# Kernel tuning notes

Hardware: AMD Instinct MI355X
Metric: run time of the kernel (lower is better)

Reference implementation:

```python
import jax, jax.numpy as jnp
import numpy as np

B, C, H, W = 8, 64, 128, 128
G, DGPG = 4, 1
GD = G * DGPG          # total deformable groups = 4
COUT = 64
KH = KW = 3
K = KH * KW            # 9 kernel locations
PAD = STR = DIL = 1
HO, WO = 128, 128      # same padding, stride 1
OFFSET_SCALE = 1.0
CDG = C // GD          # channels per deformable group = 16
CPG = C // G           # input channels per conv group = 16
KOFF = 7
POFF = 3


def dwconv7(x, w, b):
    # depthwise 7x7 conv, groups == channels; w: [C,1,7,7]
    y = jax.lax.conv_general_dilated(
        x, w, window_strides=(1, 1), padding=[(POFF, POFF), (POFF, POFF)],
        feature_group_count=C, dimension_numbers=('NCHW', 'OIHW', 'NCHW'))
    return y + b[None, :, None, None]


def gn1(x, g, b):
    # GroupNorm with a single group: normalize over (C,H,W) per sample
    m = x.mean(axis=(1, 2, 3), keepdims=True)
    v = x.var(axis=(1, 2, 3), keepdims=True)
    return (x - m) * jax.lax.rsqrt(v + 1e-5) * g[None, :, None, None] + b[None, :, None, None]


def pw(x, w, b):
    # 1x1 conv; w: [O, C]
    return jnp.einsum('bchw,oc->bohw', x, w) + b[None, :, None, None]


def setup_inputs() -> dict:
    key = jax.random.key(0)
    ks = jax.random.split(key, 8)
    s = 0.02
    return {
        'x': jax.random.normal(ks[0], (B, C, H, W), jnp.float32),
        'w_dw_off': jax.random.normal(ks[1], (C, 1, KOFF, KOFF), jnp.float32) * s,
        'b_dw_off': jnp.zeros((C,), jnp.float32),
        'gn_off_g': jnp.ones((C,), jnp.float32),
        'gn_off_b': jnp.zeros((C,), jnp.float32),
        'w_pw_off': jax.random.normal(ks[2], (GD * K * 2, C), jnp.float32) * s,
        'b_pw_off': jnp.zeros((GD * K * 2,), jnp.float32),
        'w_dw_m': jax.random.normal(ks[3], (C, 1, KOFF, KOFF), jnp.float32) * s,
        'b_dw_m': jnp.zeros((C,), jnp.float32),
        'gn_m_g': jnp.ones((C,), jnp.float32),
        'gn_m_b': jnp.zeros((C,), jnp.float32),
        'w_pw_m': jax.random.normal(ks[4], (GD * K, C), jnp.float32) * s,
        'b_pw_m': jnp.zeros((GD * K,), jnp.float32),
        'weight': jax.random.normal(ks[5], (COUT, CPG, KH, KW), jnp.float32) * s,
        'bias': jax.random.normal(ks[6], (COUT,), jnp.float32) * s,
    }


def _deform_conv(x, offset, mask, weight, bias):
    # offset: [B, GD, K, 2, HO, WO] (y, x); mask: [B, GD, K, HO, WO] (softmaxed)
    ky, kx = jnp.meshgrid(jnp.arange(KH), jnp.arange(KW), indexing='ij')
    ky = ky.reshape(K).astype(x.dtype)
    kx = kx.reshape(K).astype(x.dtype)
    oy = jnp.arange(HO, dtype=x.dtype)
    ox = jnp.arange(WO, dtype=x.dtype)
    base_y = oy[None, :] * STR - PAD + ky[:, None] * DIL   # [K, HO]
    base_x = ox[None, :] * STR - PAD + kx[:, None] * DIL   # [K, WO]
    py = base_y[None, None, :, :, None] + offset[:, :, :, 0] * OFFSET_SCALE  # [B,GD,K,HO,WO]
    px = base_x[None, None, :, None, :] + offset[:, :, :, 1] * OFFSET_SCALE

    x_flat = x.reshape(B, GD, CDG, H * W)
    y0 = jnp.floor(py)
    x0 = jnp.floor(px)
    wy = py - y0
    wx = px - x0

    def gather(yi, xi):
        valid = ((yi >= 0) & (yi < H) & (xi >= 0) & (xi < W)).astype(x.dtype)
        yc = jnp.clip(yi, 0, H - 1).astype(jnp.int32)
        xc = jnp.clip(xi, 0, W - 1).astype(jnp.int32)
        idx = (yc * W + xc).reshape(B, GD, 1, K * HO * WO)
        v = jnp.take_along_axis(x_flat, idx, axis=3).reshape(B, GD, CDG, K, HO, WO)
        return v * valid[:, :, None]

    v = (gather(y0, x0) * ((1 - wy) * (1 - wx))[:, :, None]
         + gather(y0, x0 + 1) * ((1 - wy) * wx)[:, :, None]
         + gather(y0 + 1, x0) * (wy * (1 - wx))[:, :, None]
         + gather(y0 + 1, x0 + 1) * (wy * wx)[:, :, None])
    v = v * mask[:, :, None]                               # modulated samples
    v = v.reshape(B, G, CPG, K, HO, WO)
    wg = weight.reshape(G, COUT // G, CPG, K)
    out = jnp.einsum('bgckhw,gock->bgohw', v, wg).reshape(B, COUT, HO, WO)
    return out + bias[None, :, None, None]


def reference(x, w_dw_off, b_dw_off, gn_off_g, gn_off_b, w_pw_off, b_pw_off,
              w_dw_m, b_dw_m, gn_m_g, gn_m_b, w_pw_m, b_pw_m, weight, bias):
    off = pw(gn1(dwconv7(x, w_dw_off, b_dw_off), gn_off_g, gn_off_b), w_pw_off, b_pw_off)
    m = pw(gn1(dwconv7(x, w_dw_m, b_dw_m), gn_m_g, gn_m_b), w_pw_m, b_pw_m)
    offset = off.reshape(B, GD, K, 2, HO, WO)
    mask = jax.nn.softmax(m.reshape(B, GD, K, HO, WO), axis=2)  # attn over kernel points
    return _deform_conv(x, offset, mask, weight, bias)
```

## Files before the change

kernel.cpp:

```cpp
#include <hip/hip_runtime.h>
#include <hip/hip_fp16.h>
#include <math.h>

#define HW     16384
#define IMG_H  128
#define IMG_W  128

typedef _Float16 f16x2 __attribute__((ext_vector_type(2)));
typedef __fp16 fp16v2 __attribute__((ext_vector_type(2)));
typedef _Float16 f16x4 __attribute__((ext_vector_type(4)));
typedef float f32x4 __attribute__((ext_vector_type(4)));

#define OFF_T2    ((size_t)0)
#define OFF_XT    ((size_t)8388608)
#define OFF_WT    ((size_t)12582912)
#define OFF_PART  ((size_t)12599040)
#define OFF_AD    ((size_t)12631808)
#define OFF_WB    ((size_t)19711744)
#define OFF_WDW2  ((size_t)19716352)
#define OFF_WF2   ((size_t)19719936)
#define OFF_DC    ((size_t)19775232)

__global__ void k_prep(const float* __restrict__ wpw_off,
                       const float* __restrict__ wpw_m,
                       const float* __restrict__ wdef,
                       const float* __restrict__ wdwo,
                       const float* __restrict__ wdwm,
                       float* __restrict__ ws) {
    int i = blockIdx.x * 256 + threadIdx.x;
    if (i < 6912) {
        int c = i / 108, o = i % 108;
        ws[OFF_WT + i] = (o < 72) ? wpw_off[o * 64 + c] : wpw_m[(o - 72) * 64 + c];
    } else if (i < 9216) {
        int j = i - 6912;
        int lane = j & 63;
        int gt = j >> 6;
        int tap = gt % 9, g = gt / 9;
        int oc = lane & 15, qh = lane >> 4;
        union { ushort h[4]; uint2 u; } pk;
#pragma unroll
        for (int jj = 0; jj < 4; ++jj) {
            float wv = wdef[((g * 16 + oc) * 16 + (4 * qh + jj)) * 9 + tap];
            pk.h[jj] = __half_as_ushort(__float2half(wv));
        }
        ((uint2*)(ws + OFF_WB))[j] = pk.u;
    } else if (i < 12800) {
        int j = i - 9216;
        int q = j & 3;
        int r = j >> 2;
        int dy = r % 7;
        int cv = (r / 7) & 1;
        int c = r / 14;
        const float* src = cv ? wdwm : wdwo;
        int dx0 = q * 2;
        float w0 = src[c * 49 + dy * 7 + dx0];
        float w1 = (dx0 + 1 < 7) ? src[c * 49 + dy * 7 + dx0 + 1] : 0.f;
        union { __half h[2]; uint u; } pk;
        pk.h[0] = __float2half(w0);
        pk.h[1] = __float2half(w1);
        ((uint*)(ws + OFF_WDW2))[j] = pk.u;
    }
}

__global__ __launch_bounds__(256) void k_trans(const float* __restrict__ x,
                                               __half* __restrict__ xT) {
    int n = blockIdx.x * 256 + threadIdx.x;
    int p = n & (HW - 1);
    int bg = n >> 14;
    const float* src = x + (size_t)bg * 16 * HW + p;
    union { __half2 h2[8]; uint4 u[2]; } pk;
#pragma unroll
    for (int i = 0; i < 8; ++i) {
        float a = src[(size_t)(2 * i) * HW];
        float bq = src[(size_t)(2 * i + 1) * HW];
        pk.h2[i] = __halves2half2(__float2half(a), __float2half(bq));
    }
    uint4* dst = (uint4*)(xT + (size_t)n * 16);
    dst[0] = pk.u[0];
    dst[1] = pk.u[1];
}

__global__ __launch_bounds__(256) void k_dw(const float* __restrict__ x,
                                            const float* __restrict__ bdwo,
                                            const float* __restrict__ bdwm,
                                            const uint* __restrict__ wdw2,
                                            __half2* __restrict__ t2,
                                            float* __restrict__ partial) {
    int bid = blockIdx.x;
    int plane = bid >> 4;
    int stripe = (bid & 15) * 8;
    int t = threadIdx.x;
    int cb = t & 31;
    int row = stripe + (t >> 5);
    int c = plane & 63;
    const float4* pl = (const float4*)(x + (size_t)plane * HW);

    const uint* wp = wdw2 + c * 56;
    f16x2 wo2[7][4], wm2[7][4];
    union WU { uint u; f16x2 h; };
#pragma unroll
    for (int dy = 0; dy < 7; ++dy)
#pragma unroll
        for (int q = 0; q < 4; ++q) {
            WU a, bq;
            a.u = wp[dy * 4 + q];
            bq.u = wp[28 + dy * 4 + q];
            wo2[dy][q] = a.h;
            wm2[dy][q] = bq.h;
        }

    float acco[4] = {0.f, 0.f, 0.f, 0.f};
    float accm[4] = {0.f, 0.f, 0.f, 0.f};

    union CV { fp16v2 v; f16x2 h; };

#pragma unroll
    for (int dy = 0; dy < 7; ++dy) {
        int iy = row - 3 + dy;
        if (iy >= 0 && iy < IMG_H) {
            const float4* prow = pl + iy * 32;
            float4 f4 = prow[cb];
            float4 f4m = prow[cb == 0 ? 0 : cb - 1];
            float4 f4p = prow[cb == 31 ? 31 : cb + 1];
            bool le = (cb == 0), re = (cb == 31);
            float v[11];
            v[0] = le ? 0.f : f4m.y;
            v[1] = le ? 0.f : f4m.z;
            v[2] = le ? 0.f : f4m.w;
            v[3] = f4.x; v[4] = f4.y; v[5] = f4.z; v[6] = f4.w;
            v[7] = re ? 0.f : f4p.x;
            v[8] = re ? 0.f : f4p.y;
            v[9] = re ? 0.f : f4p.z;
            v[10] = re ? 0.f : f4p.w;
            f16x2 hp[10];
#pragma unroll
            for (int d = 0; d < 10; ++d) {
                CV cv;
                cv.v = __builtin_amdgcn_cvt_pkrtz(v[d], v[d + 1]);
                hp[d] = cv.h;
            }
#pragma unroll
            for (int cc = 0; cc < 4; ++cc) {
                float ao = acco[cc], am = accm[cc];
                ao = __builtin_amdgcn_fdot2(hp[cc],     wo2[dy][0], ao, false);
                ao = __builtin_amdgcn_fdot2(hp[cc + 2], wo2[dy][1], ao, false);
                ao = __builtin_amdgcn_fdot2(hp[cc + 4], wo2[dy][2], ao, false);
                ao = __builtin_amdgcn_fdot2(hp[cc + 6], wo2[dy][3], ao, false);
                am = __builtin_amdgcn_fdot2(hp[cc],     wm2[dy][0], am, false);
                am = __builtin_amdgcn_fdot2(hp[cc + 2], wm2[dy][1], am, false);
                am = __builtin_amdgcn_fdot2(hp[cc + 4], wm2[dy][2], am, false);
                am = __builtin_amdgcn_fdot2(hp[cc + 6], wm2[dy][3], am, false);
                acco[cc] = ao; accm[cc] = am;
            }
        }
    }

    float bo = bdwo[c], bm = bdwm[c];
    float s1o = 0.f, s2o = 0.f, s1m = 0.f, s2m = 0.f;
    union { __half2 h2[4]; uint4 u; } ot;
#pragma unroll
    for (int cc = 0; cc < 4; ++cc) {
        float vo = acco[cc] + bo, vm = accm[cc] + bm;
        ot.h2[cc] = __halves2half2(__float2half(vo), __float2half(vm));
        s1o += vo; s2o += vo * vo; s1m += vm; s2m += vm * vm;
    }
    *(uint4*)(t2 + (size_t)plane * HW + row * IMG_W + cb * 4) = ot.u;

#pragma unroll
    for (int d = 32; d; d >>= 1) {
        s1o += __shfl_down(s1o, d);
        s2o += __shfl_down(s2o, d);
        s1m += __shfl_down(s1m, d);
        s2m += __shfl_down(s2m, d);
    }
    __shared__ float red[4][4];
    if ((t & 63) == 0) {
        int w = t >> 6;
        red[w][0] = s1o; red[w][1] = s2o; red[w][2] = s1m; red[w][3] = s2m;
    }
    __syncthreads();
    if (t < 4) {
        float v = red[0][t] + red[1][t] + red[2][t] + red[3][t];
        partial[(size_t)bid * 4 + t] = v;
    }
}

__global__ __launch_bounds__(256) void k_fin(const float* __restrict__ partial,
                      const float* __restrict__ gog, const float* __restrict__ gob,
                      const float* __restrict__ gmg, const float* __restrict__ gmb,
                      float* __restrict__ ad) {
    int b = blockIdx.x, t = threadIdx.x;
    const float4* pp = (const float4*)partial + (size_t)b * 1024;
    float4 s = make_float4(0.f, 0.f, 0.f, 0.f);
#pragma unroll
    for (int i = 0; i < 4; ++i) {
        float4 v = pp[t + i * 256];
        s.x += v.x; s.y += v.y; s.z += v.z; s.w += v.w;
    }
#pragma unroll
    for (int d = 32; d; d >>= 1) {
        s.x += __shfl_down(s.x, d);
        s.y += __shfl_down(s.y, d);
        s.z += __shfl_down(s.z, d);
        s.w += __shfl_down(s.w, d);
    }
    __shared__ float red[4][4];
    if ((t & 63) == 0) {
        int w = t >> 6;
        red[w][0] = s.x; red[w][1] = s.y; red[w][2] = s.z; red[w][3] = s.w;
    }
    __syncthreads();
    if (t < 64) {
        float s1o = red[0][0] + red[1][0] + red[2][0] + red[3][0];
        float s2o = red[0][1] + red[1][1] + red[2][1] + red[3][1];
        float s1m = red[0][2] + red[1][2] + red[2][2] + red[3][2];
        float s2m = red[0][3] + red[1][3] + red[2][3] + red[3][3];
        int c = t;
        const float invN = 1.f / 1048576.f;
        float m_o = s1o * invN;
        float v_o = s2o * invN - m_o * m_o;
        float i_o = rsqrtf(v_o + 1e-5f);
        float m_m = s1m * invN;
        float v_m = s2m * invN - m_m * m_m;
        float i_m = rsqrtf(v_m + 1e-5f);
        float a_o = i_o * gog[c];
        float d_o = gob[c] - m_o * a_o;
        float a_m = i_m * gmg[c];
        float d_m = gmb[c] - m_m * a_m;
        ((float4*)ad)[b * 64 + c] = make_float4(a_o, d_o, a_m, d_m);
    }
}

__global__ __launch_bounds__(256) void k_fold(const float* __restrict__ wT,
                                              const float* __restrict__ ad,
                                              const float* __restrict__ bpo,
                                              const float* __restrict__ bpm,
                                              float* __restrict__ wf2,
                                              float* __restrict__ dconst) {
    int b = blockIdx.x, t = threadIdx.x;
    const float* adb = ad + b * 256;
    for (int i = t; i < 6912; i += 256) {
        int c = i / 108, o = i - c * 108;
        float a = (o < 72) ? adb[c * 4 + 0] : adb[c * 4 + 2];
        wf2[(size_t)b * 6912 + i] = a * wT[i];
    }
    if (t < 108) {
        float s = (t < 72) ? bpo[t] : bpm[t - 72];
        for (int c = 0; c < 64; ++c) {
            float d = (t < 72) ? adb[c * 4 + 1] : adb[c * 4 + 3];
            s = fmaf(d, wT[c * 108 + t], s);
        }
        dconst[b * 108 + t] = s;
    }
}

__global__ __launch_bounds__(256, 4) void k_gthf(const __half2* __restrict__ t2,
                                                 const float* __restrict__ wf2,
                                                 const float* __restrict__ dconst,
                                                 const __half* __restrict__ xT,
                                                 const uint2* __restrict__ wb,
                                                 const float* __restrict__ bias,
                                                 float* __restrict__ out) {
    __shared__ union SMem {
        struct {
            uint4 xsA[506];
            uint4 xsB[506];
            uint4 shv[768];
        } s;
        float shout[4864];
    } sm;

    int tid = threadIdx.x;
    int bid = blockIdx.x;
    int bg = bid & 31;
    int tile = bid >> 5;
    int tr = tile >> 3, tc = tile & 7;
    int r0 = tr * 16, c0 = tc * 16;
    int g = bg & 3, b = bg >> 2;
    int wr0 = r0 - 3, wc0 = c0 - 3;

    const __half* xg = xT + (size_t)bg * HW * 16;

#pragma unroll
    for (int it = 0; it < 2; ++it) {
        int idx = tid + it * 256;
        if (idx < 484) {
            int ly = idx / 22, lx = idx - ly * 22;
            int sr = wr0 + ly; sr = sr < 0 ? 0 : (sr > 127 ? 127 : sr);
            int sc = wc0 + lx; sc = sc < 0 ? 0 : (sc > 127 ? 127 : sc);
            const uint4* src = (const uint4*)(xg + (size_t)(sr * IMG_W + sc) * 16);
            sm.s.xsA[ly * 23 + lx] = src[0];
            sm.s.xsB[ly * 23 + lx] = src[1];
        }
    }

    int row = r0 + (tid >> 4), col = c0 + (tid & 15);
    int p = row * IMG_W + col;
    int lane = tid & 63, wv = tid >> 6;
    int m_idx = lane & 15, q_idx = lane >> 4;

    const float* dc = dconst + b * 108;
    float facc[18], macc[9];
#pragma unroll
    for (int o = 0; o < 18; ++o) facc[o] = dc[g * 18 + o];
#pragma unroll
    for (int o = 0; o < 9; ++o) macc[o] = dc[72 + g * 9 + o];

    const float* wfb = wf2 + (size_t)b * 6912;
    const __half2* tp = t2 + (size_t)b * 64 * HW + p;
#pragma unroll 8
    for (int c = 0; c < 64; ++c) {
        float2 tv = __half22float2(tp[(size_t)c * HW]);
        const float* wf = wfb + c * 108 + g * 18;
#pragma unroll
        for (int o = 0; o < 18; ++o) facc[o] = fmaf(wf[o], tv.x, facc[o]);
        const float* wm = wfb + c * 108 + 72 + g * 9;
#pragma unroll
        for (int o = 0; o < 9; ++o) macc[o] = fmaf(wm[o], tv.y, macc[o]);
    }
    {
        float mx = macc[0];
#pragma unroll
        for (int k = 1; k < 9; ++k) mx = fmaxf(mx, macc[k]);
        float s = 0.f;
#pragma unroll
        for (int k = 0; k < 9; ++k) {
            float e = __expf(macc[k] - mx);
            macc[k] = e;
            s += e;
        }
        float inv = 1.f / s;
#pragma unroll
        for (int k = 0; k < 9; ++k) macc[k] *= inv;
    }

    const uint2* wbp = wb + (size_t)(g * 9) * 64 + lane;
    f16x4 bfr[9];
    union BU { uint2 u; f16x4 h; };
#pragma unroll
    for (int k = 0; k < 9; ++k) { BU t; t.u = wbp[k * 64]; bfr[k] = t.h; }

    __syncthreads();

    uint4* shvw = sm.s.shv + tid * 3;
    const _Float16* shvh = (const _Float16*)sm.s.shv;

    f32x4 acc[4];
#pragma unroll
    for (int s = 0; s < 4; ++s) acc[s] = (f32x4){0.f, 0.f, 0.f, 0.f};

#pragma unroll
    for (int k = 0; k < 9; ++k) {
        float mk = macc[k];
        float py = (float)(row + k / 3 - 1) + facc[k * 2 + 0];
        float px = (float)(col + k % 3 - 1) + facc[k * 2 + 1];
        float y0f = floorf(py), x0f = floorf(px);
        float wy = py - y0f, wx = px - x0f;
        int iy0 = (int)y0f, ix0 = (int)x0f;
        int iy1 = iy0 + 1, ix1 = ix0 + 1;
        float fy0 = (iy0 >= 0 && iy0 < IMG_H) ? (1.f - wy) : 0.f;
        float fy1 = (iy1 >= 0 && iy1 < IMG_H) ? wy : 0.f;
        float fx0 = (ix0 >= 0 && ix0 < IMG_W) ? (1.f - wx) : 0.f;
        float fx1 = (ix1 >= 0 && ix1 < IMG_W) ? wx : 0.f;
        __half2 f00h = __float2half2_rn(fy0 * fx0 * mk);
        __half2 f01h = __float2half2_rn(fy0 * fx1 * mk);
        __half2 f10h = __float2half2_rn(fy1 * fx0 * mk);
        __half2 f11h = __float2half2_rn(fy1 * fx1 * mk);
        int ly0 = iy0 - wr0; ly0 = ly0 < 0 ? 0 : (ly0 > 21 ? 21 : ly0);
        int ly1 = iy1 - wr0; ly1 = ly1 < 0 ? 0 : (ly1 > 21 ? 21 : ly1);
        int lx0 = ix0 - wc0; lx0 = lx0 < 0 ? 0 : (lx0 > 21 ? 21 : lx0);
        int lx1 = ix1 - wc0; lx1 = lx1 < 0 ? 0 : (lx1 > 21 ? 21 : lx1);
        int i00 = ly0 * 23 + lx0, i01 = ly0 * 23 + lx1;
        int i10 = ly1 * 23 + lx0, i11 = ly1 * 23 + lx1;
        union Q8 { uint4 u[2]; __half2 h2[8]; };
        Q8 q00, q01, q10, q11;
        q00.u[0] = sm.s.xsA[i00]; q00.u[1] = sm.s.xsB[i00];
        q01.u[0] = sm.s.xsA[i01]; q01.u[1] = sm.s.xsB[i01];
        q10.u[0] = sm.s.xsA[i10]; q10.u[1] = sm.s.xsB[i10];
        q11.u[0] = sm.s.xsA[i11]; q11.u[1] = sm.s.xsB[i11];
        union V8 { __half2 h2[4]; uint4 u; };
        V8 pa, pb;
#pragma unroll
        for (int i = 0; i < 4; ++i) {
            __half2 vh = __hmul2(f00h, q00.h2[i]);
            vh = __hfma2(f01h, q01.h2[i], vh);
            vh = __hfma2(f10h, q10.h2[i], vh);
            vh = __hfma2(f11h, q11.h2[i], vh);
            pa.h2[i] = vh;
        }
#pragma unroll
        for (int i = 4; i < 8; ++i) {
            __half2 vh = __hmul2(f00h, q00.h2[i]);
            vh = __hfma2(f01h, q01.h2[i], vh);
            vh = __hfma2(f10h, q10.h2[i], vh);
            vh = __hfma2(f11h, q11.h2[i], vh);
            pb.h2[i - 4] = vh;
        }
        shvw[0] = pa.u;
        shvw[1] = pb.u;
#pragma unroll
        for (int s = 0; s < 4; ++s) {
            f16x4 af = *(const f16x4*)(shvh +
                        ((size_t)wv * 64 + s * 16 + m_idx) * 24 + q_idx * 4);
            acc[s] = __builtin_amdgcn_mfma_f32_16x16x16f16(af, bfr[k], acc[s], 0, 0, 0);
        }
    }

    __syncthreads();

#pragma unroll
    for (int s = 0; s < 4; ++s)
#pragma unroll
        for (int j = 0; j < 4; ++j)
            sm.shout[(wv * 64 + s * 16 + 4 * q_idx + j) * 19 + m_idx] = acc[s][j];

    float* outp = out + ((size_t)b * 64 + g * 16) * HW + p;
#pragma unroll
    for (int o = 0; o < 16; ++o)
        outp[(size_t)o * HW] = sm.shout[tid * 19 + o] + bias[g * 16 + o];
}

extern "C" void kernel_launch(void* const* d_in, const int* in_sizes, int n_in,
                              void* d_out, int out_size, void* d_ws, size_t ws_size,
                              hipStream_t stream) {
    const float* x        = (const float*)d_in[0];
    const float* w_dw_off = (const float*)d_in[1];
    const float* b_dw_off = (const float*)d_in[2];
    const float* gn_off_g = (const float*)d_in[3];
    const float* gn_off_b = (const float*)d_in[4];
    const float* w_pw_off = (const float*)d_in[5];
    const float* b_pw_off = (const float*)d_in[6];
    const float* w_dw_m   = (const float*)d_in[7];
    const float* b_dw_m   = (const float*)d_in[8];
    const float* gn_m_g   = (const float*)d_in[9];
    const float* gn_m_b   = (const float*)d_in[10];
    const float* w_pw_m   = (const float*)d_in[11];
    const float* b_pw_m   = (const float*)d_in[12];
    const float* weight   = (const float*)d_in[13];
    const float* bias     = (const float*)d_in[14];

    float* ws = (float*)d_ws;
    __half2* t2   = (__half2*)(ws + OFF_T2);
    __half* xT    = (__half*)(ws + OFF_XT);
    float* wT     = ws + OFF_WT;
    float* part   = ws + OFF_PART;
    float* adb    = ws + OFF_AD;
    const uint2* wb = (const uint2*)(ws + OFF_WB);
    const uint* wdw2 = (const uint*)(ws + OFF_WDW2);
    float* wf2    = ws + OFF_WF2;
    float* dconst = ws + OFF_DC;

    k_prep<<<50, 256, 0, stream>>>(w_pw_off, w_pw_m, weight, w_dw_off, w_dw_m, ws);
    k_trans<<<2048, 256, 0, stream>>>(x, xT);
    k_dw<<<8192, 256, 0, stream>>>(x, b_dw_off, b_dw_m, wdw2, t2, part);
    k_fin<<<8, 256, 0, stream>>>(part, gn_off_g, gn_off_b, gn_m_g, gn_m_b, adb);
    k_fold<<<8, 256, 0, stream>>>(wT, adb, b_pw_off, b_pw_m, wf2, dconst);
    k_gthf<<<2048, 256, 0, stream>>>(t2, wf2, dconst, xT, wb, bias, (float*)d_out);
}
```

Before: 112.6 us.

## Pack channel pairs in depthwise output and use fp16 dot2 for pointwise projection

The depthwise kernel now handles two channels per block and stores the offset and mask activations with channel pairs interleaved, as fp16x2 words. The folded pointwise weights are packed as fp16 pairs in a per-(batch, group) layout. This lets the gather kernel's 64-channel projection loop run as 32 fdot2 steps instead of 64 scalar FMA steps, which halves the number of strided activation loads and weight reads. The gather block order is also changed so blocks of the same batch-group run next to each other. In exchange the folded weights lose precision by moving from fp32 to fp16, and the depthwise kernel runs half as many blocks, each doing twice the work.

```diff
diff --git a/kernel.cpp b/kernel.cpp
--- a/kernel.cpp
+++ b/kernel.cpp
@@ -18,7 +18,7 @@
 #define OFF_AD    ((size_t)12631808)
 #define OFF_WB    ((size_t)19711744)
 #define OFF_WDW2  ((size_t)19716352)
-#define OFF_WF2   ((size_t)19719936)
+#define OFF_WPK   ((size_t)19719936)
 #define OFF_DC    ((size_t)19775232)
 
 __global__ void k_prep(const float* __restrict__ wpw_off,
@@ -84,87 +84,94 @@
                                             const float* __restrict__ bdwo,
                                             const float* __restrict__ bdwm,
                                             const uint* __restrict__ wdw2,
-                                            __half2* __restrict__ t2,
+                                            uint2* __restrict__ t2p,
                                             float* __restrict__ partial) {
     int bid = blockIdx.x;
-    int plane = bid >> 4;
+    int b = bid >> 9;
+    int c2 = (bid >> 4) & 31;
     int stripe = (bid & 15) * 8;
     int t = threadIdx.x;
     int cb = t & 31;
     int row = stripe + (t >> 5);
-    int c = plane & 63;
-    const float4* pl = (const float4*)(x + (size_t)plane * HW);
-
-    const uint* wp = wdw2 + c * 56;
-    f16x2 wo2[7][4], wm2[7][4];
+    int c0 = c2 * 2;
+
+    float vo[2][4], vm[2][4];
+    float s1o = 0.f, s2o = 0.f, s1m = 0.f, s2m = 0.f;
+    union CV { fp16v2 v; f16x2 h; };
     union WU { uint u; f16x2 h; };
-#pragma unroll
-    for (int dy = 0; dy < 7; ++dy)
-#pragma unroll
-        for (int q = 0; q < 4; ++q) {
-            WU a, bq;
-            a.u = wp[dy * 4 + q];
-            bq.u = wp[28 + dy * 4 + q];
-            wo2[dy][q] = a.h;
-            wm2[dy][q] = bq.h;
-        }
-
-    float acco[4] = {0.f, 0.f, 0.f, 0.f};
-    float accm[4] = {0.f, 0.f, 0.f, 0.f};
-
-    union CV { fp16v2 v; f16x2 h; };
-
-#pragma unroll
-    for (int dy = 0; dy < 7; ++dy) {
-        int iy = row - 3 + dy;
-        if (iy >= 0 && iy < IMG_H) {
-            const float4* prow = pl + iy * 32;
-            float4 f4 = prow[cb];
-            float4 f4m = prow[cb == 0 ? 0 : cb - 1];
-            float4 f4p = prow[cb == 31 ? 31 : cb + 1];
-            bool le = (cb == 0), re = (cb == 31);
-            float v[11];
-            v[0] = le ? 0.f : f4m.y;
-            v[1] = le ? 0.f : f4m.z;
-            v[2] = le ? 0.f : f4m.w;
-            v[3] = f4.x; v[4] = f4.y; v[5] = f4.z; v[6] = f4.w;
-            v[7] = re ? 0.f : f4p.x;
-            v[8] = re ? 0.f : f4p.y;
-            v[9] = re ? 0.f : f4p.z;
-            v[10] = re ? 0.f : f4p.w;
-            f16x2 hp[10];
-#pragma unroll
-            for (int d = 0; d < 10; ++d) {
-                CV cv;
-                cv.v = __builtin_amdgcn_cvt_pkrtz(v[d], v[d + 1]);
-                hp[d] = cv.h;
+
+#pragma unroll
+    for (int ch = 0; ch < 2; ++ch) {
+        int c = c0 + ch;
+        const float4* pl = (const float4*)(x + ((size_t)(b * 64 + c)) * HW);
+        const uint* wp = wdw2 + c * 56;
+        float acco[4] = {0.f, 0.f, 0.f, 0.f};
+        float accm[4] = {0.f, 0.f, 0.f, 0.f};
+#pragma unroll
+        for (int dy = 0; dy < 7; ++dy) {
+            int iy = row - 3 + dy;
+            if (iy >= 0 && iy < IMG_H) {
+                const float4* prow = pl + iy * 32;
+                float4 f4 = prow[cb];
+                float4 f4m = prow[cb == 0 ? 0 : cb - 1];
+                float4 f4p = prow[cb == 31 ? 31 : cb + 1];
+                bool le = (cb == 0), re = (cb == 31);
+                float v[11];
+                v[0] = le ? 0.f : f4m.y;
+                v[1] = le ? 0.f : f4m.z;
+                v[2] = le ? 0.f : f4m.w;
+                v[3] = f4.x; v[4] = f4.y; v[5] = f4.z; v[6] = f4.w;
+                v[7] = re ? 0.f : f4p.x;
+                v[8] = re ? 0.f : f4p.y;
+                v[9] = re ? 0.f : f4p.z;
+                v[10] = re ? 0.f : f4p.w;
+                f16x2 hp[10];
+#pragma unroll
+                for (int d = 0; d < 10; ++d) {
+                    CV cv;
+                    cv.v = __builtin_amdgcn_cvt_pkrtz(v[d], v[d + 1]);
+                    hp[d] = cv.h;
+                }
+#pragma unroll
+                for (int cc = 0; cc < 4; ++cc) {
+                    WU w0, w1, w2, w3, u0, u1, u2, u3;
+                    w0.u = wp[dy * 4 + 0]; w1.u = wp[dy * 4 + 1];
+                    w2.u = wp[dy * 4 + 2]; w3.u = wp[dy * 4 + 3];
+                    u0.u = wp[28 + dy * 4 + 0]; u1.u = wp[28 + dy * 4 + 1];
+                    u2.u = wp[28 + dy * 4 + 2]; u3.u = wp[28 + dy * 4 + 3];
+                    float ao = acco[cc], am = accm[cc];
+                    ao = __builtin_amdgcn_fdot2(hp[cc],     w0.h, ao, false);
+                    ao = __builtin_amdgcn_fdot2(hp[cc + 2], w1.h, ao, false);
+                    ao = __builtin_amdgcn_fdot2(hp[cc + 4], w2.h, ao, false);
+                    ao = __builtin_amdgcn_fdot2(hp[cc + 6], w3.h, ao, false);
+                    am = __builtin_amdgcn_fdot2(hp[cc],     u0.h, am, false);
+                    am = __builtin_amdgcn_fdot2(hp[cc + 2], u1.h, am, false);
+                    am = __builtin_amdgcn_fdot2(hp[cc + 4], u2.h, am, false);
+                    am = __builtin_amdgcn_fdot2(hp[cc + 6], u3.h, am, false);
+                    acco[cc] = ao; accm[cc] = am;
+                }
             }
-#pragma unroll
-            for (int cc = 0; cc < 4; ++cc) {
-                float ao = acco[cc], am = accm[cc];
-                ao = __builtin_amdgcn_fdot2(hp[cc],     wo2[dy][0], ao, false);
-                ao = __builtin_amdgcn_fdot2(hp[cc + 2], wo2[dy][1], ao, false);
-                ao = __builtin_amdgcn_fdot2(hp[cc + 4], wo2[dy][2], ao, false);
-                ao = __builtin_amdgcn_fdot2(hp[cc + 6], wo2[dy][3], ao, false);
-                am = __builtin_amdgcn_fdot2(hp[cc],     wm2[dy][0], am, false);
-                am = __builtin_amdgcn_fdot2(hp[cc + 2], wm2[dy][1], am, false);
-                am = __builtin_amdgcn_fdot2(hp[cc + 4], wm2[dy][2], am, false);
-                am = __builtin_amdgcn_fdot2(hp[cc + 6], wm2[dy][3], am, false);
-                acco[cc] = ao; accm[cc] = am;
-            }
-        }
-    }
-
-    float bo = bdwo[c], bm = bdwm[c];
-    float s1o = 0.f, s2o = 0.f, s1m = 0.f, s2m = 0.f;
-    union { __half2 h2[4]; uint4 u; } ot;
+        }
+        float bo = bdwo[c], bm = bdwm[c];
+#pragma unroll
+        for (int cc = 0; cc < 4; ++cc) {
+            float o_ = acco[cc] + bo, m_ = accm[cc] + bm;
+            vo[ch][cc] = o_; vm[ch][cc] = m_;
+            s1o += o_; s2o += o_ * o_; s1m += m_; s2m += m_ * m_;
+        }
+    }
+
+    union { uint2 u2[4]; uint4 u4[2]; } ot;
 #pragma unroll
     for (int cc = 0; cc < 4; ++cc) {
-        float vo = acco[cc] + bo, vm = accm[cc] + bm;
-        ot.h2[cc] = __halves2half2(__float2half(vo), __float2half(vm));
-        s1o += vo; s2o += vo * vo; s1m += vm; s2m += vm * vm;
-    }
-    *(uint4*)(t2 + (size_t)plane * HW + row * IMG_W + cb * 4) = ot.u;
+        ot.u2[cc].x = (uint)__half_as_ushort(__float2half(vo[0][cc])) |
+                      ((uint)__half_as_ushort(__float2half(vo[1][cc])) << 16);
+        ot.u2[cc].y = (uint)__half_as_ushort(__float2half(vm[0][cc])) |
+                      ((uint)__half_as_ushort(__float2half(vm[1][cc])) << 16);
+    }
+    uint4* dst = (uint4*)(t2p + ((size_t)(b * 32 + c2) * HW + row * IMG_W + cb * 4));
+    dst[0] = ot.u4[0];
+    dst[1] = ot.u4[1];
 
 #pragma unroll
     for (int d = 32; d; d >>= 1) {
@@ -190,10 +197,10 @@
                       const float* __restrict__ gmg, const float* __restrict__ gmb,
                       float* __restrict__ ad) {
     int b = blockIdx.x, t = threadIdx.x;
-    const float4* pp = (const float4*)partial + (size_t)b * 1024;
+    const float4* pp = (const float4*)partial + (size_t)b * 512;
     float4 s = make_float4(0.f, 0.f, 0.f, 0.f);
 #pragma unroll
-    for (int i = 0; i < 4; ++i) {
+    for (int i = 0; i < 2; ++i) {
         float4 v = pp[t + i * 256];
         s.x += v.x; s.y += v.y; s.z += v.z; s.w += v.w;
     }
@@ -235,14 +242,28 @@
                                               const float* __restrict__ ad,
                                               const float* __restrict__ bpo,
                                               const float* __restrict__ bpm,
-                                              float* __restrict__ wf2,
+                                              uint* __restrict__ wpk,
                                               float* __restrict__ dconst) {
     int b = blockIdx.x, t = threadIdx.x;
     const float* adb = ad + b * 256;
-    for (int i = t; i < 6912; i += 256) {
-        int c = i / 108, o = i - c * 108;
-        float a = (o < 72) ? adb[c * 4 + 0] : adb[c * 4 + 2];
-        wf2[(size_t)b * 6912 + i] = a * wT[i];
+    for (int i = t; i < 3456; i += 256) {
+        int o27 = i % 27;
+        int c2 = (i / 27) & 31;
+        int g = i / (27 * 32);
+        int c0 = c2 * 2, c1 = c0 + 1;
+        float w0, w1;
+        if (o27 < 18) {
+            int o = g * 18 + o27;
+            w0 = adb[c0 * 4 + 0] * wT[c0 * 108 + o];
+            w1 = adb[c1 * 4 + 0] * wT[c1 * 108 + o];
+        } else {
+            int o = 72 + g * 9 + (o27 - 18);
+            w0 = adb[c0 * 4 + 2] * wT[c0 * 108 + o];
+            w1 = adb[c1 * 4 + 2] * wT[c1 * 108 + o];
+        }
+        wpk[(size_t)b * 3456 + i] =
+            (uint)__half_as_ushort(__float2half(w0)) |
+            ((uint)__half_as_ushort(__float2half(w1)) << 16);
     }
     if (t < 108) {
         float s = (t < 72) ? bpo[t] : bpm[t - 72];
@@ -254,8 +275,8 @@
     }
 }
 
-__global__ __launch_bounds__(256, 4) void k_gthf(const __half2* __restrict__ t2,
-                                                 const float* __restrict__ wf2,
+__global__ __launch_bounds__(256, 4) void k_gthf(const uint2* __restrict__ t2p,
+                                                 const uint* __restrict__ wpk,
                                                  const float* __restrict__ dconst,
                                                  const __half* __restrict__ xT,
                                                  const uint2* __restrict__ wb,
@@ -272,8 +293,8 @@
 
     int tid = threadIdx.x;
     int bid = blockIdx.x;
-    int bg = bid & 31;
-    int tile = bid >> 5;
+    int bg = bid >> 6;
+    int tile = bid & 63;
     int tr = tile >> 3, tc = tile & 7;
     int r0 = tr * 16, c0 = tc * 16;
     int g = bg & 3, b = bg >> 2;
@@ -306,17 +327,25 @@
 #pragma unroll
     for (int o = 0; o < 9; ++o) macc[o] = dc[72 + g * 9 + o];
 
-    const float* wfb = wf2 + (size_t)b * 6912;
-    const __half2* tp = t2 + (size_t)b * 64 * HW + p;
+    const uint2* tp = t2p + (size_t)b * 32 * HW + p;
+    const uint* wgp = wpk + ((size_t)(b * 4 + g)) * 32 * 27;
+    union WU { uint u; f16x2 h; };
 #pragma unroll 8
-    for (int c = 0; c < 64; ++c) {
-        float2 tv = __half22float2(tp[(size_t)c * HW]);
-        const float* wf = wfb + c * 108 + g * 18;
-#pragma unroll
-        for (int o = 0; o < 18; ++o) facc[o] = fmaf(wf[o], tv.x, facc[o]);
-        const float* wm = wfb + c * 108 + 72 + g * 9;
-#pragma unroll
-        for (int o = 0; o < 9; ++o) macc[o] = fmaf(wm[o], tv.y, macc[o]);
+    for (int c2 = 0; c2 < 32; ++c2) {
+        uint2 pk = tp[(size_t)c2 * HW];
+        WU ho, hm;
+        ho.u = pk.x; hm.u = pk.y;
+        const uint* wr = wgp + c2 * 27;
+#pragma unroll
+        for (int o = 0; o < 18; ++o) {
+            WU w; w.u = wr[o];
+            facc[o] = __builtin_amdgcn_fdot2(ho.h, w.h, facc[o], false);
+        }
+#pragma unroll
+        for (int o = 0; o < 9; ++o) {
+            WU w; w.u = wr[18 + o];
+            macc[o] = __builtin_amdgcn_fdot2(hm.h, w.h, macc[o], false);
+        }
     }
     {
         float mx = macc[0];
@@ -440,20 +469,20 @@
     const float* bias     = (const float*)d_in[14];
 
     float* ws = (float*)d_ws;
-    __half2* t2   = (__half2*)(ws + OFF_T2);
+    uint2* t2p    = (uint2*)(ws + OFF_T2);
     __half* xT    = (__half*)(ws + OFF_XT);
     float* wT     = ws + OFF_WT;
     float* part   = ws + OFF_PART;
     float* adb    = ws + OFF_AD;
     const uint2* wb = (const uint2*)(ws + OFF_WB);
     const uint* wdw2 = (const uint*)(ws + OFF_WDW2);
-    float* wf2    = ws + OFF_WF2;
+    uint* wpk     = (uint*)(ws + OFF_WPK);
     float* dconst = ws + OFF_DC;
 
     k_prep<<<50, 256, 0, stream>>>(w_pw_off, w_pw_m, weight, w_dw_off, w_dw_m, ws);
     k_trans<<<2048, 256, 0, stream>>>(x, xT);
-    k_dw<<<8192, 256, 0, stream>>>(x, b_dw_off, b_dw_m, wdw2, t2, part);
+    k_dw<<<4096, 256, 0, stream>>>(x, b_dw_off, b_dw_m, wdw2, t2p, part);
     k_fin<<<8, 256, 0, stream>>>(part, gn_off_g, gn_off_b, gn_m_g, gn_m_b, adb);
-    k_fold<<<8, 256, 0, stream>>>(wT, adb, b_pw_off, b_pw_m, wf2, dconst);
-    k_gthf<<<2048, 256, 0, stream>>>(t2, wf2, dconst, xT, wb, bias, (float*)d_out);
-}
+    k_fold<<<8, 256, 0, stream>>>(wT, adb, b_pw_off, b_pw_m, wpk, dconst);
+    k_gthf<<<2048, 256, 0, stream>>>(t2p, wpk, dconst, xT, wb, bias, (float*)d_out);
+}
```

Result: faster. 103.6 us, median of 2 (-7.9%).
